# Optimization experiments

Measured on AMD Instinct MI355X. Metric: run time of the kernel, lower is better.

The kernel has to match this reference:

```python
import jax, jax.numpy as jnp
import numpy as np

NFEATURES = 8192
NPCAS = 256
SIGMA = 16.0
COEFF_NORM = np.sqrt(NPCAS) / SIGMA  # = 1.0
FEAT_NORM = np.sqrt(2.0 / NFEATURES)
TWO_PI = 2.0 * np.pi


def fwht(x):
    """Normalized fast Walsh-Hadamard transform along the last axis (power of 2)."""
    d = x.shape[-1]
    h = 1
    while h < d:
        y = x.reshape(*x.shape[:-1], d // (2 * h), 2, h)
        a, b = y[..., 0, :], y[..., 1, :]
        x = jnp.stack([a + b, a - b], axis=-2).reshape(*x.shape)
        h *= 2
    return x * (d ** -0.5)


def setup_inputs() -> dict:
    key = jax.random.key(0)
    k = jax.random.split(key, 6)
    M, A, R = 32, 64, 512
    S = 4
    nstacks = NFEATURES // NPCAS
    rep = jax.random.normal(k[0], (M, A, R), dtype=jnp.float32)
    charges = jax.random.randint(k[1], (M, A), 0, S, dtype=jnp.int32)
    reductors = jax.random.normal(k[2], (S, R, NPCAS), dtype=jnp.float32)
    Dmat = jax.random.normal(k[3], (S, 1, nstacks, NPCAS), dtype=jnp.float32)
    bias = jax.random.uniform(k[4], (S, NFEATURES), dtype=jnp.float32) * TWO_PI
    alpha = jax.random.normal(k[5], (NFEATURES,), dtype=jnp.float32)
    return {"rep": rep, "charges": charges, "reductors": reductors,
            "Dmat": Dmat, "bias": bias, "alpha": alpha}


def reference(rep, charges, reductors, Dmat, bias, alpha):
    M, A, R = rep.shape
    S, _, P = reductors.shape
    ntransforms, nstacks = Dmat.shape[1], Dmat.shape[2]
    F = nstacks * P
    D = jnp.where(Dmat >= 0, 1.0, -1.0).astype(rep.dtype)  # +-1 SORF diagonals
    Z = jnp.zeros((M, F), dtype=rep.dtype)
    for s in range(S):
        # PCA projection: [M, A, P]
        proj = jnp.einsum('mar,rp->map', rep, reductors[s])
        # replicate across stacks: [M, A, nstacks, P]
        x = jnp.broadcast_to(proj[:, :, None, :], (M, A, nstacks, P))
        for t in range(ntransforms):
            x = fwht(D[s, t] * x)
        coeffs = COEFF_NORM * x.reshape(M, A, F)
        feats = jnp.cos(coeffs + bias[s])
        mask = (charges == s)[..., None]  # species membership per atom
        Z = Z + FEAT_NORM * jnp.sum(jnp.where(mask, feats, 0.0), axis=1)
    return Z @ alpha  # [M] out-of-sample predictions
```

## Files before the change

### kernel.cpp

```cpp
#include <hip/hip_runtime.h>

#define NATOMS 2048
#define R_DIM 512
#define P_DIM 256
#define S_DIM 4
#define NSTACKS 32
#define F_DIM 8192
#define KS 8
#define KSPAN (R_DIM / KS)
#define TR 64
#define TC 128
#define KT 16
#define RT_TILES 11

#define DPPF(x, ctrl) \
  __int_as_float(__builtin_amdgcn_update_dpp( \
      __float_as_int(x), __float_as_int(x), (ctrl), 0xF, 0xF, false))

#if defined(__has_builtin)
#if __has_builtin(__builtin_amdgcn_permlane16_swap) && \
    __has_builtin(__builtin_amdgcn_permlane32_swap)
#define HAVE_PERMLANE_SWAP 1
#endif
#endif

__device__ __forceinline__ float bfly16(float x, float sg) {
#ifdef HAVE_PERMLANE_SWAP
  auto r = __builtin_amdgcn_permlane16_swap(__float_as_uint(x), __float_as_uint(x),
                                            false, false);
  return fmaf(sg, __uint_as_float(r[1]), __uint_as_float(r[0]));
#else
  return fmaf(sg, x, __shfl_xor(x, 16));
#endif
}
__device__ __forceinline__ float bfly32(float x, float sg) {
#ifdef HAVE_PERMLANE_SWAP
  auto r = __builtin_amdgcn_permlane32_swap(__float_as_uint(x), __float_as_uint(x),
                                            false, false);
  return fmaf(sg, __uint_as_float(r[1]), __uint_as_float(r[0]));
#else
  return fmaf(sg, x, __shfl_xor(x, 32));
#endif
}
__device__ __forceinline__ float redsum16(float x) {
#ifdef HAVE_PERMLANE_SWAP
  auto r = __builtin_amdgcn_permlane16_swap(__float_as_uint(x), __float_as_uint(x),
                                            false, false);
  return __uint_as_float(r[0]) + __uint_as_float(r[1]);
#else
  return x + __shfl_xor(x, 16);
#endif
}
__device__ __forceinline__ float redsum32(float x) {
#ifdef HAVE_PERMLANE_SWAP
  auto r = __builtin_amdgcn_permlane32_swap(__float_as_uint(x), __float_as_uint(x),
                                            false, false);
  return __uint_as_float(r[0]) + __uint_as_float(r[1]);
#else
  return x + __shfl_xor(x, 32);
#endif
}


__global__ __launch_bounds__(256) void sorf_proj_kernel(
    const float* __restrict__ rep, const float* __restrict__ reductors,
    const int* __restrict__ charges, float* __restrict__ projp,
    float* __restrict__ out) {
  int bid = blockIdx.x;
  int ks = bid & 7;
  int cb = (bid >> 3) & 1;
  int r2 = bid >> 4;
  int rt = r2 % RT_TILES;
  int s  = r2 / RT_TILES;

  int t = threadIdx.x;
  int lane = t & 63, wave = t >> 6;
  if (bid == 0 && t < 32) out[t] = 0.f;

  __shared__ int rowsL[TR];
  __shared__ int wtot[4];
  int4 c0v = ((const int4*)charges)[t * 2];
  int4 c1v = ((const int4*)charges)[t * 2 + 1];
  int fl[8];
  fl[0] = (c0v.x == s); fl[1] = (c0v.y == s); fl[2] = (c0v.z == s); fl[3] = (c0v.w == s);
  fl[4] = (c1v.x == s); fl[5] = (c1v.y == s); fl[6] = (c1v.z == s); fl[7] = (c1v.w == s);
  int cnt8 = ((fl[0] + fl[1]) + (fl[2] + fl[3])) + ((fl[4] + fl[5]) + (fl[6] + fl[7]));
  int scan = cnt8;
#pragma unroll
  for (int o = 1; o < 64; o <<= 1) {
    int y = __shfl_up(scan, o);
    if (lane >= o) scan += y;
  }
  if (lane == 63) wtot[wave] = scan;
  __syncthreads();
  int wb = 0;
#pragma unroll
  for (int w = 0; w < 4; ++w) wb += (w < wave) ? wtot[w] : 0;
  int total = (wtot[0] + wtot[1]) + (wtot[2] + wtot[3]);
  int lo = rt * TR;
  int nrows = min(TR, total - lo);
  if (nrows <= 0) return;
  if (t >= nrows && t < TR) rowsL[t] = 0;
  int pos = wb + scan - cnt8;
#pragma unroll
  for (int i = 0; i < 8; ++i) {
    if (fl[i]) {
      int rel = pos - lo;
      if (rel >= 0 && rel < TR) rowsL[rel] = t * 8 + i;
      pos++;
    }
  }
  __syncthreads();

  __shared__ float As[KT][TR + 4];
  __shared__ float Bs[KT][TC];

  int ar = t >> 2;
  int aq = t & 3;
  const float* aSrc = rep + (size_t)rowsL[ar] * R_DIM + ks * KSPAN + aq * 4;
  int kb = t >> 4;
  int cc = (t & 15) * 4;
  const float* bSrc = reductors + ((size_t)s * R_DIM + ks * KSPAN + kb) * P_DIM + cb * TC + cc;

  int ty = t >> 4, tx = t & 15;
  int r0 = ty * 4;
  int c0 = tx * 4;

  float acc[4][8];
#pragma unroll
  for (int i = 0; i < 4; ++i)
#pragma unroll
    for (int j = 0; j < 8; ++j) acc[i][j] = 0.f;

  float4 a  = *(const float4*)aSrc;
  float4 b0 = *(const float4*)bSrc;
  float4 b1 = *(const float4*)(bSrc + 64);

#pragma unroll 1
  for (int k0 = 0; k0 < KSPAN; k0 += KT) {
    __syncthreads();
    As[aq * 4 + 0][ar] = a.x;
    As[aq * 4 + 1][ar] = a.y;
    As[aq * 4 + 2][ar] = a.z;
    As[aq * 4 + 3][ar] = a.w;
    *(float4*)&Bs[kb][cc] = b0;
    *(float4*)&Bs[kb][cc + 64] = b1;
    __syncthreads();
    if (k0 + KT < KSPAN) {
      a  = *(const float4*)(aSrc + k0 + KT);
      b0 = *(const float4*)(bSrc + (size_t)(k0 + KT) * P_DIM);
      b1 = *(const float4*)(bSrc + (size_t)(k0 + KT) * P_DIM + 64);
    }
#pragma unroll
    for (int kk = 0; kk < KT; ++kk) {
      float4 aV = *(const float4*)&As[kk][r0];
      float4 bA = *(const float4*)&Bs[kk][c0];
      float4 bB = *(const float4*)&Bs[kk][c0 + 64];
      float av[4] = {aV.x, aV.y, aV.z, aV.w};
      float bv[8] = {bA.x, bA.y, bA.z, bA.w, bB.x, bB.y, bB.z, bB.w};
#pragma unroll
      for (int i = 0; i < 4; ++i)
#pragma unroll
        for (int j = 0; j < 8; ++j) acc[i][j] = fmaf(av[i], bv[j], acc[i][j]);
    }
  }

#pragma unroll
  for (int i = 0; i < 4; ++i) {
    int r = r0 + i;
    if (r < nrows) {
      float* dst = projp + ((size_t)ks * NATOMS + rowsL[r]) * P_DIM + cb * TC + c0;
      *(float4*)dst = make_float4(acc[i][0], acc[i][1], acc[i][2], acc[i][3]);
      *(float4*)(dst + 64) = make_float4(acc[i][4], acc[i][5], acc[i][6], acc[i][7]);
    }
  }
}

__global__ __launch_bounds__(256) void sorf_feat_kernel(
    const float* __restrict__ projp, const int* __restrict__ charges,
    const float* __restrict__ Dmat, const float* __restrict__ bias,
    const float* __restrict__ alpha, float* __restrict__ out) {
  const int atom = blockIdx.x;
  const int t = threadIdx.x;
  const int lane = t & 63;
  const int wave = t >> 6;
  const int s = charges[atom];

  float4 p = *((const float4*)(projp + (size_t)atom * P_DIM) + lane);
#pragma unroll
  for (int ksi = 1; ksi < KS; ++ksi) {
    float4 q = *((const float4*)(projp + ((size_t)ksi * NATOMS + atom) * P_DIM) + lane);
    p.x += q.x; p.y += q.y; p.z += q.z; p.w += q.w;
  }

  const float sg1  = (lane & 1)  ? -1.f : 1.f;
  const float sg2  = (lane & 2)  ? -1.f : 1.f;
  const float sg4  = (lane & 4)  ? -1.f : 1.f;
  const float sg8  = (lane & 8)  ? -1.f : 1.f;
  const float sg16 = (lane & 16) ? -1.f : 1.f;
  const float sg32 = (lane & 32) ? -1.f : 1.f;
  const bool hi4 = (lane & 4) != 0;

  const float* Db = Dmat + (size_t)s * (NSTACKS * P_DIM);
  const float* bb = bias + (size_t)s * F_DIM;
  float accum = 0.f;

#pragma unroll 2
  for (int j = wave * 8; j < wave * 8 + 8; ++j) {
    float4 d  = *((const float4*)(Db + j * P_DIM) + lane);
    float4 bi = *((const float4*)(bb + j * P_DIM) + lane);
    float4 al = *((const float4*)(alpha + j * P_DIM) + lane);
    float x0 = (d.x >= 0.f) ? p.x : -p.x;
    float x1 = (d.y >= 0.f) ? p.y : -p.y;
    float x2 = (d.z >= 0.f) ? p.z : -p.z;
    float x3 = (d.w >= 0.f) ? p.w : -p.w;
    float t0 = x0 + x1, t1 = x0 - x1, t2 = x2 + x3, t3 = x2 - x3;
    x0 = t0 + t2; x2 = t0 - t2; x1 = t1 + t3; x3 = t1 - t3;
    { float y0 = DPPF(x0, 0xB1), y1 = DPPF(x1, 0xB1), y2 = DPPF(x2, 0xB1), y3 = DPPF(x3, 0xB1);
      x0 = fmaf(sg1, x0, y0); x1 = fmaf(sg1, x1, y1);
      x2 = fmaf(sg1, x2, y2); x3 = fmaf(sg1, x3, y3); }
    { float y0 = DPPF(x0, 0x4E), y1 = DPPF(x1, 0x4E), y2 = DPPF(x2, 0x4E), y3 = DPPF(x3, 0x4E);
      x0 = fmaf(sg2, x0, y0); x1 = fmaf(sg2, x1, y1);
      x2 = fmaf(sg2, x2, y2); x3 = fmaf(sg2, x3, y3); }
    { float a0 = DPPF(x0, 0x104), a1 = DPPF(x1, 0x104), a2 = DPPF(x2, 0x104), a3 = DPPF(x3, 0x104);
      float b0 = DPPF(x0, 0x114), b1 = DPPF(x1, 0x114), b2 = DPPF(x2, 0x114), b3 = DPPF(x3, 0x114);
      float y0 = hi4 ? b0 : a0;
      float y1 = hi4 ? b1 : a1;
      float y2 = hi4 ? b2 : a2;
      float y3 = hi4 ? b3 : a3;
      x0 = fmaf(sg4, x0, y0); x1 = fmaf(sg4, x1, y1);
      x2 = fmaf(sg4, x2, y2); x3 = fmaf(sg4, x3, y3); }
    { float y0 = DPPF(x0, 0x128), y1 = DPPF(x1, 0x128), y2 = DPPF(x2, 0x128), y3 = DPPF(x3, 0x128);
      x0 = fmaf(sg8, x0, y0); x1 = fmaf(sg8, x1, y1);
      x2 = fmaf(sg8, x2, y2); x3 = fmaf(sg8, x3, y3); }
    x0 = bfly16(x0, sg16); x1 = bfly16(x1, sg16);
    x2 = bfly16(x2, sg16); x3 = bfly16(x3, sg16);
    x0 = bfly32(x0, sg32); x1 = bfly32(x1, sg32);
    x2 = bfly32(x2, sg32); x3 = bfly32(x3, sg32);
    accum += __cosf(fmaf(x0, 0.0625f, bi.x)) * al.x;
    accum += __cosf(fmaf(x1, 0.0625f, bi.y)) * al.y;
    accum += __cosf(fmaf(x2, 0.0625f, bi.z)) * al.z;
    accum += __cosf(fmaf(x3, 0.0625f, bi.w)) * al.w;
  }

  accum += DPPF(accum, 0xB1);
  accum += DPPF(accum, 0x4E);
  accum += DPPF(accum, 0x124);
  accum += DPPF(accum, 0x128);
  accum = redsum16(accum);
  accum = redsum32(accum);

  __shared__ float wsum[4];
  if (lane == 0) wsum[wave] = accum;
  __syncthreads();
  if (t == 0) {
    atomicAdd(out + (atom >> 6), 0.015625f * ((wsum[0] + wsum[1]) + (wsum[2] + wsum[3])));
  }
}

extern "C" void kernel_launch(void* const* d_in, const int* in_sizes, int n_in,
                              void* d_out, int out_size, void* d_ws, size_t ws_size,
                              hipStream_t stream) {
  const float* rep       = (const float*)d_in[0];
  const int*   charges   = (const int*)d_in[1];
  const float* reductors = (const float*)d_in[2];
  const float* Dmat      = (const float*)d_in[3];
  const float* bias      = (const float*)d_in[4];
  const float* alpha     = (const float*)d_in[5];
  float* out = (float*)d_out;

  float* projp = (float*)((char*)d_ws + 16384);

  sorf_proj_kernel<<<8 * 2 * RT_TILES * S_DIM, 256, 0, stream>>>(
      rep, reductors, charges, projp, out);
  sorf_feat_kernel<<<NATOMS, 256, 0, stream>>>(projp, charges, Dmat, bias, alpha, out);
}
```

Baseline: 111.4 us.

## Process two same-species atoms per block in feature kernel to reuse Dmat/bias/alpha loads

The projection kernel now records each species' atom count and a sorted list of atom indices in the workspace. The feature kernel launches blocks per species pair slot, so each block handles two atoms of the same species. This lets one set of Dmat, bias and alpha loads, and the per-block overhead, serve both atoms. The cost is about double the register use per thread and some idle blocks that return early for slots past each species' count. It also depends on the RT_TILES*TR capacity of 704 atoms per species.

Measured after the change: 103.2 us. 7.3% less time.

```diff
diff --git a/kernel.cpp b/kernel.cpp
--- a/kernel.cpp
+++ b/kernel.cpp
@@ -12,6 +12,8 @@
 #define TC 128
 #define KT 16
 #define RT_TILES 11
+#define SORT_PITCH (RT_TILES * TR)
+#define PAIRS_PER_S (SORT_PITCH / 2)
 
 #define DPPF(x, ctrl) \
   __int_as_float(__builtin_amdgcn_update_dpp( \
@@ -65,6 +67,7 @@
 __global__ __launch_bounds__(256) void sorf_proj_kernel(
     const float* __restrict__ rep, const float* __restrict__ reductors,
     const int* __restrict__ charges, float* __restrict__ projp,
+    int* __restrict__ scnt, int* __restrict__ sorted,
     float* __restrict__ out) {
   int bid = blockIdx.x;
   int ks = bid & 7;
@@ -97,6 +100,7 @@
 #pragma unroll
   for (int w = 0; w < 4; ++w) wb += (w < wave) ? wtot[w] : 0;
   int total = (wtot[0] + wtot[1]) + (wtot[2] + wtot[3]);
+  if (ks == 0 && cb == 0 && rt == 0 && t == 0) scnt[s] = total;
   int lo = rt * TR;
   int nrows = min(TR, total - lo);
   if (nrows <= 0) return;
@@ -111,6 +115,7 @@
     }
   }
   __syncthreads();
+  if (ks == 0 && cb == 0 && t < nrows) sorted[s * SORT_PITCH + lo + t] = rowsL[t];
 
   __shared__ float As[KT][TR + 4];
   __shared__ float Bs[KT][TC];
@@ -177,20 +182,31 @@
 }
 
 __global__ __launch_bounds__(256) void sorf_feat_kernel(
-    const float* __restrict__ projp, const int* __restrict__ charges,
-    const float* __restrict__ Dmat, const float* __restrict__ bias,
-    const float* __restrict__ alpha, float* __restrict__ out) {
-  const int atom = blockIdx.x;
+    const float* __restrict__ projp, const int* __restrict__ scnt,
+    const int* __restrict__ sorted, const float* __restrict__ Dmat,
+    const float* __restrict__ bias, const float* __restrict__ alpha,
+    float* __restrict__ out) {
+  const int s  = blockIdx.x / PAIRS_PER_S;
+  const int pr = blockIdx.x % PAIRS_PER_S;
+  const int cntS = scnt[s];
+  const int slot0 = pr * 2;
+  if (slot0 >= cntS) return;
+  const bool v1 = (slot0 + 1) < cntS;
+  const int atom0 = sorted[s * SORT_PITCH + slot0];
+  const int atom1 = v1 ? sorted[s * SORT_PITCH + slot0 + 1] : atom0;
+
   const int t = threadIdx.x;
   const int lane = t & 63;
   const int wave = t >> 6;
-  const int s = charges[atom];
-
-  float4 p = *((const float4*)(projp + (size_t)atom * P_DIM) + lane);
+
+  float4 p0 = *((const float4*)(projp + (size_t)atom0 * P_DIM) + lane);
+  float4 p1 = *((const float4*)(projp + (size_t)atom1 * P_DIM) + lane);
 #pragma unroll
   for (int ksi = 1; ksi < KS; ++ksi) {
-    float4 q = *((const float4*)(projp + ((size_t)ksi * NATOMS + atom) * P_DIM) + lane);
-    p.x += q.x; p.y += q.y; p.z += q.z; p.w += q.w;
+    float4 q0 = *((const float4*)(projp + ((size_t)ksi * NATOMS + atom0) * P_DIM) + lane);
+    float4 q1 = *((const float4*)(projp + ((size_t)ksi * NATOMS + atom1) * P_DIM) + lane);
+    p0.x += q0.x; p0.y += q0.y; p0.z += q0.z; p0.w += q0.w;
+    p1.x += q1.x; p1.y += q1.y; p1.z += q1.z; p1.w += q1.w;
   }
 
   const float sg1  = (lane & 1)  ? -1.f : 1.f;
@@ -203,25 +219,37 @@
 
   const float* Db = Dmat + (size_t)s * (NSTACKS * P_DIM);
   const float* bb = bias + (size_t)s * F_DIM;
-  float accum = 0.f;
+  float accum0 = 0.f, accum1 = 0.f;
 
 #pragma unroll 2
   for (int j = wave * 8; j < wave * 8 + 8; ++j) {
     float4 d  = *((const float4*)(Db + j * P_DIM) + lane);
     float4 bi = *((const float4*)(bb + j * P_DIM) + lane);
     float4 al = *((const float4*)(alpha + j * P_DIM) + lane);
-    float x0 = (d.x >= 0.f) ? p.x : -p.x;
-    float x1 = (d.y >= 0.f) ? p.y : -p.y;
-    float x2 = (d.z >= 0.f) ? p.z : -p.z;
-    float x3 = (d.w >= 0.f) ? p.w : -p.w;
-    float t0 = x0 + x1, t1 = x0 - x1, t2 = x2 + x3, t3 = x2 - x3;
-    x0 = t0 + t2; x2 = t0 - t2; x1 = t1 + t3; x3 = t1 - t3;
+    float x0 = (d.x >= 0.f) ? p0.x : -p0.x;
+    float x1 = (d.y >= 0.f) ? p0.y : -p0.y;
+    float x2 = (d.z >= 0.f) ? p0.z : -p0.z;
+    float x3 = (d.w >= 0.f) ? p0.w : -p0.w;
+    float u0 = (d.x >= 0.f) ? p1.x : -p1.x;
+    float u1 = (d.y >= 0.f) ? p1.y : -p1.y;
+    float u2 = (d.z >= 0.f) ? p1.z : -p1.z;
+    float u3 = (d.w >= 0.f) ? p1.w : -p1.w;
+    { float t0 = x0 + x1, t1 = x0 - x1, t2 = x2 + x3, t3 = x2 - x3;
+      x0 = t0 + t2; x2 = t0 - t2; x1 = t1 + t3; x3 = t1 - t3; }
+    { float t0 = u0 + u1, t1 = u0 - u1, t2 = u2 + u3, t3 = u2 - u3;
+      u0 = t0 + t2; u2 = t0 - t2; u1 = t1 + t3; u3 = t1 - t3; }
     { float y0 = DPPF(x0, 0xB1), y1 = DPPF(x1, 0xB1), y2 = DPPF(x2, 0xB1), y3 = DPPF(x3, 0xB1);
+      float z0 = DPPF(u0, 0xB1), z1 = DPPF(u1, 0xB1), z2 = DPPF(u2, 0xB1), z3 = DPPF(u3, 0xB1);
       x0 = fmaf(sg1, x0, y0); x1 = fmaf(sg1, x1, y1);
-      x2 = fmaf(sg1, x2, y2); x3 = fmaf(sg1, x3, y3); }
+      x2 = fmaf(sg1, x2, y2); x3 = fmaf(sg1, x3, y3);
+      u0 = fmaf(sg1, u0, z0); u1 = fmaf(sg1, u1, z1);
+      u2 = fmaf(sg1, u2, z2); u3 = fmaf(sg1, u3, z3); }
     { float y0 = DPPF(x0, 0x4E), y1 = DPPF(x1, 0x4E), y2 = DPPF(x2, 0x4E), y3 = DPPF(x3, 0x4E);
+      float z0 = DPPF(u0, 0x4E), z1 = DPPF(u1, 0x4E), z2 = DPPF(u2, 0x4E), z3 = DPPF(u3, 0x4E);
       x0 = fmaf(sg2, x0, y0); x1 = fmaf(sg2, x1, y1);
-      x2 = fmaf(sg2, x2, y2); x3 = fmaf(sg2, x3, y3); }
+      x2 = fmaf(sg2, x2, y2); x3 = fmaf(sg2, x3, y3);
+      u0 = fmaf(sg2, u0, z0); u1 = fmaf(sg2, u1, z1);
+      u2 = fmaf(sg2, u2, z2); u3 = fmaf(sg2, u3, z3); }
     { float a0 = DPPF(x0, 0x104), a1 = DPPF(x1, 0x104), a2 = DPPF(x2, 0x104), a3 = DPPF(x3, 0x104);
       float b0 = DPPF(x0, 0x114), b1 = DPPF(x1, 0x114), b2 = DPPF(x2, 0x114), b3 = DPPF(x3, 0x114);
       float y0 = hi4 ? b0 : a0;
@@ -230,31 +258,60 @@
       float y3 = hi4 ? b3 : a3;
       x0 = fmaf(sg4, x0, y0); x1 = fmaf(sg4, x1, y1);
       x2 = fmaf(sg4, x2, y2); x3 = fmaf(sg4, x3, y3); }
+    { float a0 = DPPF(u0, 0x104), a1 = DPPF(u1, 0x104), a2 = DPPF(u2, 0x104), a3 = DPPF(u3, 0x104);
+      float b0 = DPPF(u0, 0x114), b1 = DPPF(u1, 0x114), b2 = DPPF(u2, 0x114), b3 = DPPF(u3, 0x114);
+      float z0 = hi4 ? b0 : a0;
+      float z1 = hi4 ? b1 : a1;
+      float z2 = hi4 ? b2 : a2;
+      float z3 = hi4 ? b3 : a3;
+      u0 = fmaf(sg4, u0, z0); u1 = fmaf(sg4, u1, z1);
+      u2 = fmaf(sg4, u2, z2); u3 = fmaf(sg4, u3, z3); }
     { float y0 = DPPF(x0, 0x128), y1 = DPPF(x1, 0x128), y2 = DPPF(x2, 0x128), y3 = DPPF(x3, 0x128);
+      float z0 = DPPF(u0, 0x128), z1 = DPPF(u1, 0x128), z2 = DPPF(u2, 0x128), z3 = DPPF(u3, 0x128);
       x0 = fmaf(sg8, x0, y0); x1 = fmaf(sg8, x1, y1);
-      x2 = fmaf(sg8, x2, y2); x3 = fmaf(sg8, x3, y3); }
+      x2 = fmaf(sg8, x2, y2); x3 = fmaf(sg8, x3, y3);
+      u0 = fmaf(sg8, u0, z0); u1 = fmaf(sg8, u1, z1);
+      u2 = fmaf(sg8, u2, z2); u3 = fmaf(sg8, u3, z3); }
     x0 = bfly16(x0, sg16); x1 = bfly16(x1, sg16);
     x2 = bfly16(x2, sg16); x3 = bfly16(x3, sg16);
+    u0 = bfly16(u0, sg16); u1 = bfly16(u1, sg16);
+    u2 = bfly16(u2, sg16); u3 = bfly16(u3, sg16);
     x0 = bfly32(x0, sg32); x1 = bfly32(x1, sg32);
     x2 = bfly32(x2, sg32); x3 = bfly32(x3, sg32);
-    accum += __cosf(fmaf(x0, 0.0625f, bi.x)) * al.x;
-    accum += __cosf(fmaf(x1, 0.0625f, bi.y)) * al.y;
-    accum += __cosf(fmaf(x2, 0.0625f, bi.z)) * al.z;
-    accum += __cosf(fmaf(x3, 0.0625f, bi.w)) * al.w;
-  }
-
-  accum += DPPF(accum, 0xB1);
-  accum += DPPF(accum, 0x4E);
-  accum += DPPF(accum, 0x124);
-  accum += DPPF(accum, 0x128);
-  accum = redsum16(accum);
-  accum = redsum32(accum);
-
-  __shared__ float wsum[4];
-  if (lane == 0) wsum[wave] = accum;
+    u0 = bfly32(u0, sg32); u1 = bfly32(u1, sg32);
+    u2 = bfly32(u2, sg32); u3 = bfly32(u3, sg32);
+    accum0 += __cosf(fmaf(x0, 0.0625f, bi.x)) * al.x;
+    accum0 += __cosf(fmaf(x1, 0.0625f, bi.y)) * al.y;
+    accum0 += __cosf(fmaf(x2, 0.0625f, bi.z)) * al.z;
+    accum0 += __cosf(fmaf(x3, 0.0625f, bi.w)) * al.w;
+    accum1 += __cosf(fmaf(u0, 0.0625f, bi.x)) * al.x;
+    accum1 += __cosf(fmaf(u1, 0.0625f, bi.y)) * al.y;
+    accum1 += __cosf(fmaf(u2, 0.0625f, bi.z)) * al.z;
+    accum1 += __cosf(fmaf(u3, 0.0625f, bi.w)) * al.w;
+  }
+
+  accum0 += DPPF(accum0, 0xB1);
+  accum0 += DPPF(accum0, 0x4E);
+  accum0 += DPPF(accum0, 0x124);
+  accum0 += DPPF(accum0, 0x128);
+  accum0 = redsum16(accum0);
+  accum0 = redsum32(accum0);
+  accum1 += DPPF(accum1, 0xB1);
+  accum1 += DPPF(accum1, 0x4E);
+  accum1 += DPPF(accum1, 0x124);
+  accum1 += DPPF(accum1, 0x128);
+  accum1 = redsum16(accum1);
+  accum1 = redsum32(accum1);
+
+  __shared__ float wsum0[4], wsum1[4];
+  if (lane == 0) { wsum0[wave] = accum0; wsum1[wave] = accum1; }
   __syncthreads();
   if (t == 0) {
-    atomicAdd(out + (atom >> 6), 0.015625f * ((wsum[0] + wsum[1]) + (wsum[2] + wsum[3])));
+    atomicAdd(out + (atom0 >> 6),
+              0.015625f * ((wsum0[0] + wsum0[1]) + (wsum0[2] + wsum0[3])));
+    if (v1)
+      atomicAdd(out + (atom1 >> 6),
+                0.015625f * ((wsum1[0] + wsum1[1]) + (wsum1[2] + wsum1[3])));
   }
 }
 
@@ -269,9 +326,12 @@
   const float* alpha     = (const float*)d_in[5];
   float* out = (float*)d_out;
 
-  float* projp = (float*)((char*)d_ws + 16384);
+  int*   scnt   = (int*)d_ws;
+  int*   sorted = (int*)((char*)d_ws + 64);
+  float* projp  = (float*)((char*)d_ws + 16384);
 
   sorf_proj_kernel<<<8 * 2 * RT_TILES * S_DIM, 256, 0, stream>>>(
-      rep, reductors, charges, projp, out);
-  sorf_feat_kernel<<<NATOMS, 256, 0, stream>>>(projp, charges, Dmat, bias, alpha, out);
-}
+      rep, reductors, charges, projp, scnt, sorted, out);
+  sorf_feat_kernel<<<S_DIM * PAIRS_PER_S, 256, 0, stream>>>(
+      projp, scnt, sorted, Dmat, bias, alpha, out);
+}
```

## Group atoms by species so feature blocks process four atoms sharing SORF tables

Applied to the files above, without the earlier changes.

The projection kernel now records per-species atom counts and a species-sorted atom list. The feature kernel uses these so each block handles four same-species atoms, loading the Dmat, bias and alpha rows once and reusing them across four transform chains. This cuts table traffic and block count, at the cost of more registers per thread and some idle blocks when a species has fewer atoms than its padded slots. The projection GEMM K-tile is also doubled to 32, which halves the synchronisations per tile.

Measured after the change: 111.7 us. Within noise of the previous version (+0.2%).

```diff
diff --git a/kernel.cpp b/kernel.cpp
--- a/kernel.cpp
+++ b/kernel.cpp
@@ -10,8 +10,10 @@
 #define KSPAN (R_DIM / KS)
 #define TR 64
 #define TC 128
-#define KT 16
+#define KT 32
 #define RT_TILES 11
+#define SORT_PITCH (RT_TILES * TR)
+#define QUADS_PER_S (SORT_PITCH / 4)
 
 #define DPPF(x, ctrl) \
   __int_as_float(__builtin_amdgcn_update_dpp( \
@@ -61,10 +63,48 @@
 #endif
 }
 
+__device__ __forceinline__ float chain8(float4 p, float4 d, float4 bi, float4 al,
+                                        float sg1, float sg2, float sg4, float sg8,
+                                        float sg16, float sg32, bool hi4) {
+  float x0 = (d.x >= 0.f) ? p.x : -p.x;
+  float x1 = (d.y >= 0.f) ? p.y : -p.y;
+  float x2 = (d.z >= 0.f) ? p.z : -p.z;
+  float x3 = (d.w >= 0.f) ? p.w : -p.w;
+  { float t0 = x0 + x1, t1 = x0 - x1, t2 = x2 + x3, t3 = x2 - x3;
+    x0 = t0 + t2; x2 = t0 - t2; x1 = t1 + t3; x3 = t1 - t3; }
+  { float y0 = DPPF(x0, 0xB1), y1 = DPPF(x1, 0xB1), y2 = DPPF(x2, 0xB1), y3 = DPPF(x3, 0xB1);
+    x0 = fmaf(sg1, x0, y0); x1 = fmaf(sg1, x1, y1);
+    x2 = fmaf(sg1, x2, y2); x3 = fmaf(sg1, x3, y3); }
+  { float y0 = DPPF(x0, 0x4E), y1 = DPPF(x1, 0x4E), y2 = DPPF(x2, 0x4E), y3 = DPPF(x3, 0x4E);
+    x0 = fmaf(sg2, x0, y0); x1 = fmaf(sg2, x1, y1);
+    x2 = fmaf(sg2, x2, y2); x3 = fmaf(sg2, x3, y3); }
+  { float a0 = DPPF(x0, 0x104), a1 = DPPF(x1, 0x104), a2 = DPPF(x2, 0x104), a3 = DPPF(x3, 0x104);
+    float b0 = DPPF(x0, 0x114), b1 = DPPF(x1, 0x114), b2 = DPPF(x2, 0x114), b3 = DPPF(x3, 0x114);
+    float y0 = hi4 ? b0 : a0;
+    float y1 = hi4 ? b1 : a1;
+    float y2 = hi4 ? b2 : a2;
+    float y3 = hi4 ? b3 : a3;
+    x0 = fmaf(sg4, x0, y0); x1 = fmaf(sg4, x1, y1);
+    x2 = fmaf(sg4, x2, y2); x3 = fmaf(sg4, x3, y3); }
+  { float y0 = DPPF(x0, 0x128), y1 = DPPF(x1, 0x128), y2 = DPPF(x2, 0x128), y3 = DPPF(x3, 0x128);
+    x0 = fmaf(sg8, x0, y0); x1 = fmaf(sg8, x1, y1);
+    x2 = fmaf(sg8, x2, y2); x3 = fmaf(sg8, x3, y3); }
+  x0 = bfly16(x0, sg16); x1 = bfly16(x1, sg16);
+  x2 = bfly16(x2, sg16); x3 = bfly16(x3, sg16);
+  x0 = bfly32(x0, sg32); x1 = bfly32(x1, sg32);
+  x2 = bfly32(x2, sg32); x3 = bfly32(x3, sg32);
+  float r = __cosf(fmaf(x0, 0.0625f, bi.x)) * al.x;
+  r += __cosf(fmaf(x1, 0.0625f, bi.y)) * al.y;
+  r += __cosf(fmaf(x2, 0.0625f, bi.z)) * al.z;
+  r += __cosf(fmaf(x3, 0.0625f, bi.w)) * al.w;
+  return r;
+}
+
 
 __global__ __launch_bounds__(256) void sorf_proj_kernel(
     const float* __restrict__ rep, const float* __restrict__ reductors,
     const int* __restrict__ charges, float* __restrict__ projp,
+    int* __restrict__ scnt, int* __restrict__ sorted,
     float* __restrict__ out) {
   int bid = blockIdx.x;
   int ks = bid & 7;
@@ -97,6 +137,7 @@
 #pragma unroll
   for (int w = 0; w < 4; ++w) wb += (w < wave) ? wtot[w] : 0;
   int total = (wtot[0] + wtot[1]) + (wtot[2] + wtot[3]);
+  if (ks == 0 && cb == 0 && rt == 0 && t == 0) scnt[s] = total;
   int lo = rt * TR;
   int nrows = min(TR, total - lo);
   if (nrows <= 0) return;
@@ -111,6 +152,7 @@
     }
   }
   __syncthreads();
+  if (ks == 0 && cb == 0 && t < nrows) sorted[s * SORT_PITCH + lo + t] = rowsL[t];
 
   __shared__ float As[KT][TR + 4];
   __shared__ float Bs[KT][TC];
@@ -132,24 +174,36 @@
 #pragma unroll
     for (int j = 0; j < 8; ++j) acc[i][j] = 0.f;
 
-  float4 a  = *(const float4*)aSrc;
-  float4 b0 = *(const float4*)bSrc;
-  float4 b1 = *(const float4*)(bSrc + 64);
+  float4 a0  = *(const float4*)aSrc;
+  float4 a1  = *(const float4*)(aSrc + 16);
+  float4 b00 = *(const float4*)bSrc;
+  float4 b01 = *(const float4*)(bSrc + 64);
+  float4 b10 = *(const float4*)(bSrc + 16 * P_DIM);
+  float4 b11 = *(const float4*)(bSrc + 16 * P_DIM + 64);
 
 #pragma unroll 1
   for (int k0 = 0; k0 < KSPAN; k0 += KT) {
     __syncthreads();
-    As[aq * 4 + 0][ar] = a.x;
-    As[aq * 4 + 1][ar] = a.y;
-    As[aq * 4 + 2][ar] = a.z;
-    As[aq * 4 + 3][ar] = a.w;
-    *(float4*)&Bs[kb][cc] = b0;
-    *(float4*)&Bs[kb][cc + 64] = b1;
+    As[aq * 4 + 0][ar] = a0.x;
+    As[aq * 4 + 1][ar] = a0.y;
+    As[aq * 4 + 2][ar] = a0.z;
+    As[aq * 4 + 3][ar] = a0.w;
+    As[16 + aq * 4 + 0][ar] = a1.x;
+    As[16 + aq * 4 + 1][ar] = a1.y;
+    As[16 + aq * 4 + 2][ar] = a1.z;
+    As[16 + aq * 4 + 3][ar] = a1.w;
+    *(float4*)&Bs[kb][cc]           = b00;
+    *(float4*)&Bs[kb][cc + 64]      = b01;
+    *(float4*)&Bs[kb + 16][cc]      = b10;
+    *(float4*)&Bs[kb + 16][cc + 64] = b11;
     __syncthreads();
     if (k0 + KT < KSPAN) {
-      a  = *(const float4*)(aSrc + k0 + KT);
-      b0 = *(const float4*)(bSrc + (size_t)(k0 + KT) * P_DIM);
-      b1 = *(const float4*)(bSrc + (size_t)(k0 + KT) * P_DIM + 64);
+      a0  = *(const float4*)(aSrc + k0 + KT);
+      a1  = *(const float4*)(aSrc + k0 + KT + 16);
+      b00 = *(const float4*)(bSrc + (size_t)(k0 + KT) * P_DIM);
+      b01 = *(const float4*)(bSrc + (size_t)(k0 + KT) * P_DIM + 64);
+      b10 = *(const float4*)(bSrc + (size_t)(k0 + KT + 16) * P_DIM);
+      b11 = *(const float4*)(bSrc + (size_t)(k0 + KT + 16) * P_DIM + 64);
     }
 #pragma unroll
     for (int kk = 0; kk < KT; ++kk) {
@@ -177,20 +231,43 @@
 }
 
 __global__ __launch_bounds__(256) void sorf_feat_kernel(
-    const float* __restrict__ projp, const int* __restrict__ charges,
-    const float* __restrict__ Dmat, const float* __restrict__ bias,
-    const float* __restrict__ alpha, float* __restrict__ out) {
-  const int atom = blockIdx.x;
+    const float* __restrict__ projp, const int* __restrict__ scnt,
+    const int* __restrict__ sorted, const float* __restrict__ Dmat,
+    const float* __restrict__ bias, const float* __restrict__ alpha,
+    float* __restrict__ out) {
+  const int s = blockIdx.x / QUADS_PER_S;
+  const int q = blockIdx.x % QUADS_PER_S;
+  const int cntS = scnt[s];
+  const int slot0 = q * 4;
+  if (slot0 >= cntS) return;
+  const bool v1 = (slot0 + 1) < cntS;
+  const bool v2 = (slot0 + 2) < cntS;
+  const bool v3 = (slot0 + 3) < cntS;
+  const int base = s * SORT_PITCH + slot0;
+  const int at0 = sorted[base];
+  const int at1 = v1 ? sorted[base + 1] : at0;
+  const int at2 = v2 ? sorted[base + 2] : at0;
+  const int at3 = v3 ? sorted[base + 3] : at0;
+
   const int t = threadIdx.x;
   const int lane = t & 63;
   const int wave = t >> 6;
-  const int s = charges[atom];
-
-  float4 p = *((const float4*)(projp + (size_t)atom * P_DIM) + lane);
+
+  float4 p0 = *((const float4*)(projp + (size_t)at0 * P_DIM) + lane);
+  float4 p1 = *((const float4*)(projp + (size_t)at1 * P_DIM) + lane);
+  float4 p2 = *((const float4*)(projp + (size_t)at2 * P_DIM) + lane);
+  float4 p3 = *((const float4*)(projp + (size_t)at3 * P_DIM) + lane);
 #pragma unroll
   for (int ksi = 1; ksi < KS; ++ksi) {
-    float4 q = *((const float4*)(projp + ((size_t)ksi * NATOMS + atom) * P_DIM) + lane);
-    p.x += q.x; p.y += q.y; p.z += q.z; p.w += q.w;
+    const size_t o = (size_t)ksi * NATOMS;
+    float4 q0 = *((const float4*)(projp + (o + at0) * P_DIM) + lane);
+    float4 q1 = *((const float4*)(projp + (o + at1) * P_DIM) + lane);
+    float4 q2 = *((const float4*)(projp + (o + at2) * P_DIM) + lane);
+    float4 q3 = *((const float4*)(projp + (o + at3) * P_DIM) + lane);
+    p0.x += q0.x; p0.y += q0.y; p0.z += q0.z; p0.w += q0.w;
+    p1.x += q1.x; p1.y += q1.y; p1.z += q1.z; p1.w += q1.w;
+    p2.x += q2.x; p2.y += q2.y; p2.z += q2.z; p2.w += q2.w;
+    p3.x += q3.x; p3.y += q3.y; p3.z += q3.z; p3.w += q3.w;
   }
 
   const float sg1  = (lane & 1)  ? -1.f : 1.f;
@@ -203,58 +280,50 @@
 
   const float* Db = Dmat + (size_t)s * (NSTACKS * P_DIM);
   const float* bb = bias + (size_t)s * F_DIM;
-  float accum = 0.f;
+  float accum0 = 0.f, accum1 = 0.f, accum2 = 0.f, accum3 = 0.f;
 
 #pragma unroll 2
   for (int j = wave * 8; j < wave * 8 + 8; ++j) {
     float4 d  = *((const float4*)(Db + j * P_DIM) + lane);
     float4 bi = *((const float4*)(bb + j * P_DIM) + lane);
     float4 al = *((const float4*)(alpha + j * P_DIM) + lane);
-    float x0 = (d.x >= 0.f) ? p.x : -p.x;
-    float x1 = (d.y >= 0.f) ? p.y : -p.y;
-    float x2 = (d.z >= 0.f) ? p.z : -p.z;
-    float x3 = (d.w >= 0.f) ? p.w : -p.w;
-    float t0 = x0 + x1, t1 = x0 - x1, t2 = x2 + x3, t3 = x2 - x3;
-    x0 = t0 + t2; x2 = t0 - t2; x1 = t1 + t3; x3 = t1 - t3;
-    { float y0 = DPPF(x0, 0xB1), y1 = DPPF(x1, 0xB1), y2 = DPPF(x2, 0xB1), y3 = DPPF(x3, 0xB1);
-      x0 = fmaf(sg1, x0, y0); x1 = fmaf(sg1, x1, y1);
-      x2 = fmaf(sg1, x2, y2); x3 = fmaf(sg1, x3, y3); }
-    { float y0 = DPPF(x0, 0x4E), y1 = DPPF(x1, 0x4E), y2 = DPPF(x2, 0x4E), y3 = DPPF(x3, 0x4E);
-      x0 = fmaf(sg2, x0, y0); x1 = fmaf(sg2, x1, y1);
-      x2 = fmaf(sg2, x2, y2); x3 = fmaf(sg2, x3, y3); }
-    { float a0 = DPPF(x0, 0x104), a1 = DPPF(x1, 0x104), a2 = DPPF(x2, 0x104), a3 = DPPF(x3, 0x104);
-      float b0 = DPPF(x0, 0x114), b1 = DPPF(x1, 0x114), b2 = DPPF(x2, 0x114), b3 = DPPF(x3, 0x114);
-      float y0 = hi4 ? b0 : a0;
-      float y1 = hi4 ? b1 : a1;
-      float y2 = hi4 ? b2 : a2;
-      float y3 = hi4 ? b3 : a3;
-      x0 = fmaf(sg4, x0, y0); x1 = fmaf(sg4, x1, y1);
-      x2 = fmaf(sg4, x2, y2); x3 = fmaf(sg4, x3, y3); }
-    { float y0 = DPPF(x0, 0x128), y1 = DPPF(x1, 0x128), y2 = DPPF(x2, 0x128), y3 = DPPF(x3, 0x128);
-      x0 = fmaf(sg8, x0, y0); x1 = fmaf(sg8, x1, y1);
-      x2 = fmaf(sg8, x2, y2); x3 = fmaf(sg8, x3, y3); }
-    x0 = bfly16(x0, sg16); x1 = bfly16(x1, sg16);
-    x2 = bfly16(x2, sg16); x3 = bfly16(x3, sg16);
-    x0 = bfly32(x0, sg32); x1 = bfly32(x1, sg32);
-    x2 = bfly32(x2, sg32); x3 = bfly32(x3, sg32);
-    accum += __cosf(fmaf(x0, 0.0625f, bi.x)) * al.x;
-    accum += __cosf(fmaf(x1, 0.0625f, bi.y)) * al.y;
-    accum += __cosf(fmaf(x2, 0.0625f, bi.z)) * al.z;
-    accum += __cosf(fmaf(x3, 0.0625f, bi.w)) * al.w;
-  }
-
-  accum += DPPF(accum, 0xB1);
-  accum += DPPF(accum, 0x4E);
-  accum += DPPF(accum, 0x124);
-  accum += DPPF(accum, 0x128);
-  accum = redsum16(accum);
-  accum = redsum32(accum);
-
-  __shared__ float wsum[4];
-  if (lane == 0) wsum[wave] = accum;
+    accum0 += chain8(p0, d, bi, al, sg1, sg2, sg4, sg8, sg16, sg32, hi4);
+    accum1 += chain8(p1, d, bi, al, sg1, sg2, sg4, sg8, sg16, sg32, hi4);
+    accum2 += chain8(p2, d, bi, al, sg1, sg2, sg4, sg8, sg16, sg32, hi4);
+    accum3 += chain8(p3, d, bi, al, sg1, sg2, sg4, sg8, sg16, sg32, hi4);
+  }
+
+  accum0 += DPPF(accum0, 0xB1); accum0 += DPPF(accum0, 0x4E);
+  accum0 += DPPF(accum0, 0x124); accum0 += DPPF(accum0, 0x128);
+  accum0 = redsum16(accum0); accum0 = redsum32(accum0);
+  accum1 += DPPF(accum1, 0xB1); accum1 += DPPF(accum1, 0x4E);
+  accum1 += DPPF(accum1, 0x124); accum1 += DPPF(accum1, 0x128);
+  accum1 = redsum16(accum1); accum1 = redsum32(accum1);
+  accum2 += DPPF(accum2, 0xB1); accum2 += DPPF(accum2, 0x4E);
+  accum2 += DPPF(accum2, 0x124); accum2 += DPPF(accum2, 0x128);
+  accum2 = redsum16(accum2); accum2 = redsum32(accum2);
+  accum3 += DPPF(accum3, 0xB1); accum3 += DPPF(accum3, 0x4E);
+  accum3 += DPPF(accum3, 0x124); accum3 += DPPF(accum3, 0x128);
+  accum3 = redsum16(accum3); accum3 = redsum32(accum3);
+
+  __shared__ float wsum[4][4];
+  if (lane == 0) {
+    wsum[wave][0] = accum0; wsum[wave][1] = accum1;
+    wsum[wave][2] = accum2; wsum[wave][3] = accum3;
+  }
   __syncthreads();
   if (t == 0) {
-    atomicAdd(out + (atom >> 6), 0.015625f * ((wsum[0] + wsum[1]) + (wsum[2] + wsum[3])));
+    atomicAdd(out + (at0 >> 6),
+              0.015625f * ((wsum[0][0] + wsum[1][0]) + (wsum[2][0] + wsum[3][0])));
+    if (v1)
+      atomicAdd(out + (at1 >> 6),
+                0.015625f * ((wsum[0][1] + wsum[1][1]) + (wsum[2][1] + wsum[3][1])));
+    if (v2)
+      atomicAdd(out + (at2 >> 6),
+                0.015625f * ((wsum[0][2] + wsum[1][2]) + (wsum[2][2] + wsum[3][2])));
+    if (v3)
+      atomicAdd(out + (at3 >> 6),
+                0.015625f * ((wsum[0][3] + wsum[1][3]) + (wsum[2][3] + wsum[3][3])));
   }
 }
 
@@ -269,9 +338,12 @@
   const float* alpha     = (const float*)d_in[5];
   float* out = (float*)d_out;
 
-  float* projp = (float*)((char*)d_ws + 16384);
-
-  sorf_proj_kernel<<<8 * 2 * RT_TILES * S_DIM, 256, 0, stream>>>(
-      rep, reductors, charges, projp, out);
-  sorf_feat_kernel<<<NATOMS, 256, 0, stream>>>(projp, charges, Dmat, bias, alpha, out);
-}
+  int*   scnt   = (int*)d_ws;
+  int*   sorted = (int*)((char*)d_ws + 64);
+  float* projp  = (float*)((char*)d_ws + 16384);
+
+  sorf_proj_kernel<<<KS * 2 * RT_TILES * S_DIM, 256, 0, stream>>>(
+      rep, reductors, charges, projp, scnt, sorted, out);
+  sorf_feat_kernel<<<S_DIM * QUADS_PER_S, 256, 0, stream>>>(
+      projp, scnt, sorted, Dmat, bias, alpha, out);
+}
```
